# Kernel tuning notes

Measured on AMD Instinct MI355X. Metric: run time of the kernel, lower is better.

## Reference

```python
import jax, jax.numpy as jnp
from jax import lax
import numpy as np

DN = ('NCHW', 'OIHW', 'NCHW')

def lecun_tanh(z):
    return 1.7159 * jnp.tanh(0.666 * z)

def setup_inputs() -> dict:
    key = jax.random.key(0)
    ks = jax.random.split(key, 20)
    s = 0.02  # small init scale for numerical sanity
    inp = {
        'x_vis': jax.random.normal(ks[0], (32, 64, 3, 64, 64), jnp.float32),
        'hx': jnp.zeros((32, 64), jnp.float32),
        'conv1_w': jax.random.normal(ks[1], (32, 3, 4, 4), jnp.float32) * s,
        'conv1_b': jax.random.normal(ks[2], (32,), jnp.float32) * s,
        'conv2_w': jax.random.normal(ks[3], (64, 32, 4, 4), jnp.float32) * s,
        'conv2_b': jax.random.normal(ks[4], (64,), jnp.float32) * s,
        'bb_w': jax.random.normal(ks[5], (16448, 128), jnp.float32) * s,
        'bb_b': jax.random.normal(ks[6], (128,), jnp.float32) * s,
        'ff1_w': jax.random.normal(ks[7], (128, 64), jnp.float32) * s,
        'ff1_b': jax.random.normal(ks[8], (64,), jnp.float32) * s,
        'ff2_w': jax.random.normal(ks[9], (128, 64), jnp.float32) * s,
        'ff2_b': jax.random.normal(ks[10], (64,), jnp.float32) * s,
        'ta_w': jax.random.normal(ks[11], (128, 64), jnp.float32) * s,
        'ta_b': jax.random.normal(ks[12], (64,), jnp.float32) * s,
        'tb_w': jax.random.normal(ks[13], (128, 64), jnp.float32) * s,
        'tb_b': jax.random.normal(ks[14], (64,), jnp.float32) * s,
        'out_w': jax.random.normal(ks[15], (64, 8), jnp.float32) * s,
        'out_b': jax.random.normal(ks[16], (8,), jnp.float32) * s,
    }
    return inp

def reference(x_vis, hx, conv1_w, conv1_b, conv2_w, conv2_b, bb_w, bb_b,
              ff1_w, ff1_b, ff2_w, ff2_b, ta_w, ta_b, tb_w, tb_b, out_w, out_b):
    B, T, C, H, W = x_vis.shape
    x = x_vis.reshape(B * T, C, H, W)
    # Visual cortex: two stride-2 convs, k=4, p=1, ReLU
    x = jax.nn.relu(lax.conv_general_dilated(x, conv1_w, (2, 2), [(1, 1), (1, 1)],
                                             dimension_numbers=DN) + conv1_b[None, :, None, None])
    x = jax.nn.relu(lax.conv_general_dilated(x, conv2_w, (2, 2), [(1, 1), (1, 1)],
                                             dimension_numbers=DN) + conv2_b[None, :, None, None])
    feats = x.reshape(B, T, -1)  # (B, T, 16384)

    # CfC liquid core (ncps default mode, backbone_units=128, ts=1.0)
    ts = jnp.float32(1.0)
    def step(h, x_t):
        z = jnp.concatenate([x_t, h], axis=-1)            # (B, 16448)
        bb = lecun_tanh(z @ bb_w + bb_b)                   # (B, 128)
        ff1 = jnp.tanh(bb @ ff1_w + ff1_b)
        ff2 = jnp.tanh(bb @ ff2_w + ff2_b)
        t_interp = jax.nn.sigmoid((bb @ ta_w + ta_b) * ts + (bb @ tb_w + tb_b))
        h_new = ff1 * (1.0 - t_interp) + t_interp * ff2
        return h_new, h_new

    new_hx, outs = lax.scan(step, hx, jnp.swapaxes(feats, 0, 1))  # outs: (T, B, 64)
    r_out = jnp.swapaxes(outs, 0, 1)                               # (B, T, 64)
    logits = r_out @ out_w + out_b                                 # (B, T, 8)
    return logits, new_hx
```

## Files before the change

kernel.cpp:

```cpp
#include <hip/hip_runtime.h>
#include <stdint.h>


typedef unsigned short u16;
typedef unsigned int u32;

typedef float f32x4 __attribute__((ext_vector_type(4)));
typedef short s16x8 __attribute__((ext_vector_type(8)));
typedef __bf16 b16x8 __attribute__((ext_vector_type(8)));

template <typename V>
__device__ inline auto mfma_sel(V a, V b, f32x4 c, int)
    -> decltype(__builtin_amdgcn_mfma_f32_16x16x32_bf16(a, b, c, 0, 0, 0)) {
  return __builtin_amdgcn_mfma_f32_16x16x32_bf16(a, b, c, 0, 0, 0);
}
template <typename V>
__device__ inline f32x4 mfma_sel(V a, V b, f32x4 c, long) {
  union UU { V s; b16x8 b; };
  UU ua; ua.s = a;
  UU ub; ub.s = b;
  return __builtin_amdgcn_mfma_f32_16x16x32_bf16(ua.b, ub.b, c, 0, 0, 0);
}
__device__ inline f32x4 mfma16x16x32(s16x8 a, s16x8 b, f32x4 c) {
  return mfma_sel(a, b, c, 0);
}

__device__ inline float bf2f(u16 v) {
  union { u32 i; float f; } x; x.i = ((u32)v) << 16; return x.f;
}
__device__ inline u16 f2bf(float f) {
  union { float f; u32 i; } x; x.f = f;
  u32 i = x.i;
  i += 0x7fffu + ((i >> 16) & 1u);
  return (u16)(i >> 16);
}
__device__ inline void bf2x2(u32 u, float& lo, float& hi) {
  union { u32 i; float f; } a, b;
  a.i = u << 16; b.i = u & 0xffff0000u;
  lo = a.f; hi = b.f;
}
__device__ inline float ldf(int isbf, const void* p, size_t i) {
  return isbf ? bf2f(((const u16*)p)[i]) : ((const float*)p)[i];
}
__device__ inline u16 ldb(int isbf, const void* p, size_t i) {
  return isbf ? ((const u16*)p)[i] : f2bf(((const float*)p)[i]);
}
__device__ inline float fast_tanh(float x) {
  float ax = fabsf(x);
  float e = __expf(2.0f * ax);
  float t = 1.0f - 2.0f / (e + 1.0f);
  return copysignf(t, x);
}

__global__ __launch_bounds__(256)
void k_prep_all(const u32* __restrict__ bwords,
                const void* b1, const void* b2, const void* bbb,
                const void* f1b, const void* f2b, const void* tab,
                const void* tbb, const void* oww, const void* obb,
                const void* hx, const void* w1, const void* w2,
                const void* bw, const void* f1w, const void* f2w,
                const void* taw, const void* tbw,
                float* __restrict__ consts, u16* __restrict__ w1p,
                u16* __restrict__ w2c, u16* __restrict__ bbT,
                u16* __restrict__ HT, int* __restrict__ flag) {
  __shared__ u16 t[64][65];
  const int tid = threadIdx.x;
  const int b = blockIdx.x;
  const u32 wd = bwords[tid & 63];
  const u32 ex = (wd >> 7) & 0xFFu;
  unsigned long long m = __ballot(ex >= 100u && ex <= 126u);
  const int isbf = (__popcll(m) >= 32) ? 1 : 0;
  if (b == 0 && tid == 0) *flag = isbf;

  if (b < 12) {
    const int e = b * 256 + tid;
    if (e >= 3048) return;
    float v;
    if (e < 32)        v = ldf(isbf, b1, e);
    else if (e < 96)   v = ldf(isbf, b2, e - 32);
    else if (e < 224)  v = ldf(isbf, bbb, e - 96);
    else if (e < 288)  v = ldf(isbf, f1b, e - 224);
    else if (e < 352)  v = ldf(isbf, f2b, e - 288);
    else if (e < 416)  v = ldf(isbf, tab, e - 352);
    else if (e < 480)  v = ldf(isbf, tbb, e - 416);
    else if (e < 992)  v = ldf(isbf, oww, e - 480);
    else if (e < 1000) v = ldf(isbf, obb, e - 992);
    else               v = ldf(isbf, hx, e - 1000);
    consts[e] = v;
  } else if (b < 20) {
    const int e = (b - 12) * 256 + tid;
    const int k = e & 63, co = e >> 6;
    w1p[e] = (k < 48) ? ldb(isbf, w1, co * 48 + k) : (u16)0;
  } else if (b < 148) {
    const int e = (b - 20) * 256 + tid;
    w2c[e] = ldb(isbf, w2, e);
  } else if (b < 662) {
    const int idx = b - 148;
    const int k0 = (idx >> 1) * 64, j0 = (idx & 1) * 64;
    #pragma unroll
    for (int i = 0; i < 16; ++i) {
      int e = tid + 256 * i;
      int kl = e >> 6, jl = e & 63;
      t[kl][jl] = ldb(isbf, bw, (size_t)(k0 + kl) * 128 + j0 + jl);
    }
    __syncthreads();
    #pragma unroll
    for (int i = 0; i < 16; ++i) {
      int e = tid + 256 * i;
      int jl = e >> 6, kl = e & 63;
      bbT[(size_t)(j0 + jl) * 16448 + k0 + kl] = t[kl][jl];
    }
  } else {
    const int idx = b - 662;
    const int h = idx >> 1, i0 = (idx & 1) * 64;
    const void* W = (h == 0) ? f1w : (h == 1) ? f2w : (h == 2) ? taw : tbw;
    #pragma unroll
    for (int i = 0; i < 16; ++i) {
      int e = tid + 256 * i;
      int il = e >> 6, cl = e & 63;
      t[il][cl] = ldb(isbf, W, (i0 + il) * 64 + cl);
    }
    __syncthreads();
    #pragma unroll
    for (int i = 0; i < 16; ++i) {
      int e = tid + 256 * i;
      int cl = e >> 6, il = e & 63;
      HT[(h * 64 + cl) * 128 + i0 + il] = t[il][cl];
    }
  }
}

__global__ __launch_bounds__(512, 4)
void k_convs(const int* __restrict__ flagp, const void* __restrict__ x,
             const u16* __restrict__ w1p, const u16* __restrict__ w2c,
             const float* __restrict__ consts, u16* __restrict__ feats) {
  __shared__ u32 lx[16592];
  const int isbf = *flagp;
  const int n = blockIdx.x;
  const int tid = threadIdx.x;
  const int wv = tid >> 6, lane = tid & 63, quad = lane >> 4, l15 = lane & 15;

  for (int e = tid; e < 10064; e += 512) {
    int idx;
    if (e < 204) {
      const int pl = e / 68;
      const int rem = e - pl * 68;
      const int r = rem / 34;
      idx = pl * 2244 + r * (65 * 34) + (rem - r * 34);
    } else if (e < 272) {
      idx = 6732 + (e - 204);
    } else {
      idx = 6800 + (e - 272);
    }
    lx[idx] = 0u;
  }
  for (int e = tid; e < 3072; e += 512) {
    const int ci = e >> 10;
    const int rr = (e >> 4) & 63;
    const int tt = e & 15;
    u32* dst = &lx[(ci * 66 + rr + 1) * 34];
    if (!isbf) {
      const float* src = (const float*)x + (((size_t)n * 3 + ci) * 64 + rr) * 64 + 4 * tt;
      const f32x4 v = *(const f32x4*)src;
      const float pv = tt ? src[-1] : 0.f;
      dst[2 * tt]     = (u32)f2bf(pv)   | (((u32)f2bf(v[0])) << 16);
      dst[2 * tt + 1] = (u32)f2bf(v[1]) | (((u32)f2bf(v[2])) << 16);
      if (tt == 15) { dst[32] = (u32)f2bf(v[3]); dst[33] = 0u; }
    } else {
      const u16* src = (const u16*)x + (((size_t)n * 3 + ci) * 64 + rr) * 64 + 4 * tt;
      const u16 pv = tt ? src[-1] : (u16)0;
      dst[2 * tt]     = (u32)pv | (((u32)src[0]) << 16);
      dst[2 * tt + 1] = (u32)src[1] | (((u32)src[2]) << 16);
      if (tt == 15) { dst[32] = (u32)src[3]; dst[33] = 0u; }
    }
  }
  __syncthreads();

  f32x4 acc2[8];
  #pragma unroll
  for (int rr = 0; rr < 8; ++rr) acc2[rr] = f32x4{0.f, 0.f, 0.f, 0.f};

  const int khb = (quad & 1) * 2;
  const int cih = quad >> 1;
  const int mt = wv & 3;
  const int og = wv >> 2;
  u16* lp = (u16*)lx;

  #pragma unroll
  for (int h = 0; h < 2; ++h) {
    const s16x8 af0 = *(const s16x8*)(w1p + (h * 16 + l15) * 64 + quad * 8);
    const s16x8 af1 = *(const s16x8*)(w1p + (h * 16 + l15) * 64 + 32 + quad * 8);
    #pragma unroll
    for (int i = 0; i < 8; ++i) {
      const int nt = wv * 8 + i;
      const int oh = nt >> 1;
      const int ob = (nt & 1) * 16;
      f32x4 a1acc = f32x4{0.f, 0.f, 0.f, 0.f};
      {
        const int base = (cih * 66 + 2 * oh + khb) * 34 + ob + l15;
        union { u32 u[4]; s16x8 v; } bf;
        bf.u[0] = lx[base];
        bf.u[1] = lx[base + 1];
        bf.u[2] = lx[base + 34];
        bf.u[3] = lx[base + 35];
        a1acc = mfma16x16x32(af0, bf.v, a1acc);
      }
      {
        const int ci1 = 2 + cih;
        const int base = (ci1 < 3) ? ((ci1 * 66 + 2 * oh + khb) * 34 + ob + l15)
                                   : (6732 + ob + l15);
        union { u32 u[4]; s16x8 v; } bf;
        bf.u[0] = lx[base];
        bf.u[1] = lx[base + 1];
        bf.u[2] = lx[base + 34];
        bf.u[3] = lx[base + 35];
        a1acc = mfma16x16x32(af1, bf.v, a1acc);
      }
      #pragma unroll
      for (int r = 0; r < 4; ++r) {
        const int co = quad * 4 + r;
        float v = a1acc[r] + consts[h * 16 + co];
        v = v > 0.f ? v : 0.f;
        lp[(6800 + (co * 34 + oh + 1) * 18) * 2 + ob + l15 + 1] = f2bf(v);
      }
    }
    __syncthreads();
    #pragma unroll
    for (int kst = 0; kst < 8; ++kst) {
      const int kglob = h * 8 + kst;
      const s16x8 afr =
          *(const s16x8*)(w2c + (mt * 16 + l15) * 512 + kglob * 32 + quad * 8);
      const int ci = kst * 2 + cih;
      #pragma unroll
      for (int rr = 0; rr < 8; ++rr) {
        const int row1 = 2 * (og * 8 + rr) + khb;
        const int base = 6800 + (ci * 34 + row1) * 18 + l15;
        union { u32 u[4]; s16x8 v; } bf;
        bf.u[0] = lx[base];
        bf.u[1] = lx[base + 1];
        bf.u[2] = lx[base + 18];
        bf.u[3] = lx[base + 19];
        acc2[rr] = mfma16x16x32(afr, bf.v, acc2[rr]);
      }
    }
    if (h == 0) __syncthreads();
  }
  #pragma unroll
  for (int rr = 0; rr < 8; ++rr) {
    const int oh = og * 8 + rr;
    #pragma unroll
    for (int r = 0; r < 4; ++r) {
      const int co = mt * 16 + quad * 4 + r;
      const float bias = consts[32 + co];
      float v = acc2[rr][r] + bias;
      v = v > 0.f ? v : 0.f;
      feats[(size_t)n * 16384 + co * 256 + oh * 16 + l15] = f2bf(v);
    }
  }
}

__global__ __launch_bounds__(256)
void k_xb(const u16* __restrict__ feats, const u16* __restrict__ bbT,
          float* __restrict__ xbp) {
  const int m0 = blockIdx.x * 64;
  const int kc = blockIdx.y;
  const int kc0 = kc * 1024;
  const int tid = threadIdx.x;
  const int w = tid >> 6, lane = tid & 63, quad = lane >> 4, l15 = lane & 15;
  f32x4 acc[4][2];
  #pragma unroll
  for (int mt = 0; mt < 4; ++mt)
    #pragma unroll
    for (int i = 0; i < 2; ++i) acc[mt][i] = f32x4{0.f, 0.f, 0.f, 0.f};
  #pragma unroll 4
  for (int kst = 0; kst < 32; ++kst) {
    const int k = kc0 + kst * 32 + quad * 8;
    s16x8 afrag[4], bfrag[2];
    #pragma unroll
    for (int mt = 0; mt < 4; ++mt)
      afrag[mt] = *(const s16x8*)(feats + (size_t)(m0 + mt * 16 + l15) * 16384 + k);
    #pragma unroll
    for (int i = 0; i < 2; ++i)
      bfrag[i] = *(const s16x8*)(bbT + (size_t)((w * 2 + i) * 16 + l15) * 16448 + k);
    #pragma unroll
    for (int mt = 0; mt < 4; ++mt)
      #pragma unroll
      for (int i = 0; i < 2; ++i)
        acc[mt][i] = mfma16x16x32(afrag[mt], bfrag[i], acc[mt][i]);
  }
  float* dst = xbp + (size_t)kc * 262144;
  #pragma unroll
  for (int mt = 0; mt < 4; ++mt)
    #pragma unroll
    for (int i = 0; i < 2; ++i) {
      const int j = (w * 2 + i) * 16 + l15;
      #pragma unroll
      for (int r = 0; r < 4; ++r) {
        const int m = m0 + mt * 16 + quad * 4 + r;
        dst[m * 128 + j] = acc[mt][i][r];
      }
    }
}

__global__ __launch_bounds__(256)
void k_xbsum(const float* __restrict__ xbp, float* __restrict__ xb) {
  const int e = blockIdx.x * 256 + threadIdx.x;
  float s = 0.f;
  #pragma unroll
  for (int kc = 0; kc < 16; ++kc) s += xbp[(size_t)kc * 262144 + e];
  xb[e] = s;
}

__global__ __launch_bounds__(256, 1)
void k_rec(const int* __restrict__ flagp, const float* __restrict__ xb,
           const u16* __restrict__ bbT, const u16* __restrict__ HT,
           const float* __restrict__ consts, float* __restrict__ rout,
           void* __restrict__ outv) {
  __shared__ float xbl[64 * 128];
  __shared__ float h[64];
  __shared__ float bbv[128];
  __shared__ float heads[256];
  const int isbf = *flagp;
  const int b = blockIdx.x;
  const int tid = threadIdx.x;
  {
    const float* src = xb + (size_t)b * 64 * 128;
    #pragma unroll
    for (int q = 0; q < 32; ++q) xbl[q * 256 + tid] = src[q * 256 + tid];
  }
  float w1r[64];
  if (tid < 128) {
    const u32* src = (const u32*)(bbT + (size_t)tid * 16448 + 16384);
    #pragma unroll
    for (int q = 0; q < 32; ++q) bf2x2(src[q], w1r[2 * q], w1r[2 * q + 1]);
  }
  float w2r[128];
  {
    const u32* src = (const u32*)(HT + tid * 128);
    #pragma unroll
    for (int q = 0; q < 64; ++q) bf2x2(src[q], w2r[2 * q], w2r[2 * q + 1]);
  }
  const float hbias = consts[224 + tid];
  const float bbias = (tid < 128) ? consts[96 + tid] : 0.f;
  if (tid < 64) h[tid] = consts[1000 + b * 64 + tid];
  __syncthreads();
  for (int t = 0; t < 64; ++t) {
    if (tid < 128) {
      float p0 = 0.f, p1 = 0.f, p2 = 0.f, p3 = 0.f;
      #pragma unroll
      for (int q = 0; q < 16; ++q) {
        p0 += h[4 * q + 0] * w1r[4 * q + 0];
        p1 += h[4 * q + 1] * w1r[4 * q + 1];
        p2 += h[4 * q + 2] * w1r[4 * q + 2];
        p3 += h[4 * q + 3] * w1r[4 * q + 3];
      }
      const float s = (p0 + p1) + (p2 + p3) + xbl[t * 128 + tid] + bbias;
      bbv[tid] = 1.7159f * fast_tanh(0.666f * s);
    }
    __syncthreads();
    float c0 = 0.f, c1 = 0.f, c2 = 0.f, c3 = 0.f;
    #pragma unroll
    for (int q = 0; q < 32; ++q) {
      c0 += bbv[4 * q + 0] * w2r[4 * q + 0];
      c1 += bbv[4 * q + 1] * w2r[4 * q + 1];
      c2 += bbv[4 * q + 2] * w2r[4 * q + 2];
      c3 += bbv[4 * q + 3] * w2r[4 * q + 3];
    }
    heads[tid] = (c0 + c1) + (c2 + c3) + hbias;
    __syncthreads();
    if (tid < 64) {
      const float ff1 = fast_tanh(heads[tid]);
      const float ff2 = fast_tanh(heads[64 + tid]);
      const float ti = 1.f / (1.f + __expf(-(heads[128 + tid] + heads[192 + tid])));
      const float hn = ff1 * (1.f - ti) + ti * ff2;
      h[tid] = hn;
      rout[((size_t)b * 64 + t) * 64 + tid] = hn;
    }
    __syncthreads();
  }
  if (tid < 64) {
    if (isbf) ((u16*)outv)[16384 + b * 64 + tid] = f2bf(h[tid]);
    else      ((float*)outv)[16384 + b * 64 + tid] = h[tid];
  }
}

__global__ __launch_bounds__(256)
void k_logits(const int* __restrict__ flagp, const float* __restrict__ rout,
              const float* __restrict__ consts, void* __restrict__ outv) {
  __shared__ float W[512];
  __shared__ float Bv[8];
  const int isbf = *flagp;
  const int tid = threadIdx.x;
  for (int e = tid; e < 512; e += 256) W[e] = consts[480 + e];
  if (tid < 8) Bv[tid] = consts[992 + tid];
  __syncthreads();
  const int bt = blockIdx.x * 256 + tid;
  float acc[8];
  #pragma unroll
  for (int c = 0; c < 8; ++c) acc[c] = Bv[c];
  const f32x4* r = (const f32x4*)(rout + (size_t)bt * 64);
  #pragma unroll
  for (int q = 0; q < 16; ++q) {
    f32x4 v = r[q];
    #pragma unroll
    for (int u = 0; u < 4; ++u) {
      const float rv = v[u];
      const int i = 4 * q + u;
      #pragma unroll
      for (int c = 0; c < 8; ++c) acc[c] += rv * W[i * 8 + c];
    }
  }
  if (isbf) {
    u32 pk[4];
    #pragma unroll
    for (int c = 0; c < 4; ++c)
      pk[c] = (u32)f2bf(acc[2 * c]) | ((u32)f2bf(acc[2 * c + 1]) << 16);
    *(uint4*)((u16*)outv + (size_t)bt * 8) = *(const uint4*)pk;
  } else {
    float* o = (float*)outv + (size_t)bt * 8;
    *(f32x4*)o = f32x4{acc[0], acc[1], acc[2], acc[3]};
    *(f32x4*)(o + 4) = f32x4{acc[4], acc[5], acc[6], acc[7]};
  }
}

extern "C" void kernel_launch(void* const* d_in, const int* in_sizes, int n_in,
                              void* d_out, int out_size, void* d_ws, size_t ws_size,
                              hipStream_t stream) {
  const void* x   = d_in[0];
  const void* hx  = d_in[1];
  const void* w1  = d_in[2];
  const void* b1  = d_in[3];
  const void* w2  = d_in[4];
  const void* b2  = d_in[5];
  const void* bbw = d_in[6];
  const void* bbb = d_in[7];
  const void* f1w = d_in[8];
  const void* f1b = d_in[9];
  const void* f2w = d_in[10];
  const void* f2b = d_in[11];
  const void* taw = d_in[12];
  const void* tab = d_in[13];
  const void* tbw = d_in[14];
  const void* tbb = d_in[15];
  const void* oww = d_in[16];
  const void* obb = d_in[17];

  char* ws = (char*)d_ws;
  float* xbp   = (float*)(ws);
  u16*   feats = (u16*)(ws + 150994944);
  u16*   bbT   = (u16*)(ws + 218103808);
  u16*   HT    = (u16*)(ws + 222314496);
  u16*   w1p   = (u16*)(ws + 222380032);
  u16*   w2c   = (u16*)(ws + 222384128);
  float* xb    = (float*)(ws + 222449664);
  float* rout  = (float*)(ws + 223498240);
  float* consts= (float*)(ws + 224022528);
  int*   flag  = (int*)(ws + 224034816);

  k_prep_all<<<670, 256, 0, stream>>>((const u32*)bbw, b1, b2, bbb, f1b, f2b,
                                      tab, tbb, oww, obb, hx, w1, w2, bbw,
                                      f1w, f2w, taw, tbw,
                                      consts, w1p, w2c, bbT, HT, flag);
  k_convs<<<2048, 512, 0, stream>>>(flag, x, w1p, w2c, consts, feats);
  k_xb<<<dim3(32, 16), 256, 0, stream>>>(feats, bbT, xbp);
  k_xbsum<<<1024, 256, 0, stream>>>(xbp, xb);
  k_rec<<<32, 256, 0, stream>>>(flag, xb, bbT, HT, consts, rout, d_out);
  k_logits<<<8, 256, 0, stream>>>(flag, rout, consts, d_out);
}
```

Baseline: 422.6 us.

## Split recurrent matvecs across 512 threads with shuffle reductions, removing a barrier

The sequential recurrence kernel now uses 512 threads per batch row. Each thread computes a partial dot product over a slice of K, and the partials are combined with cross-lane shuffles instead of one thread looping over the full K. The four head outputs are gathered by shuffles within a wave, which removes the shared heads array and one __syncthreads per timestep. This aims to shorten the serial per-step latency of the 64-step loop, at the cost of extra shuffle traffic and vectorized LDS reads.

```diff
diff --git a/kernel.cpp b/kernel.cpp
--- a/kernel.cpp
+++ b/kernel.cpp
@@ -311,70 +311,90 @@
   xb[e] = s;
 }
 
-__global__ __launch_bounds__(256, 1)
+__global__ __launch_bounds__(512, 1)
 void k_rec(const int* __restrict__ flagp, const float* __restrict__ xb,
            const u16* __restrict__ bbT, const u16* __restrict__ HT,
            const float* __restrict__ consts, float* __restrict__ rout,
            void* __restrict__ outv) {
   __shared__ float xbl[64 * 128];
-  __shared__ float h[64];
-  __shared__ float bbv[128];
-  __shared__ float heads[256];
+  __shared__ f32x4 h4[16];
+  __shared__ f32x4 bb4[32];
   const int isbf = *flagp;
   const int b = blockIdx.x;
   const int tid = threadIdx.x;
+  const int w = tid >> 6;
+  const int l = tid & 63;
+  float* h = (float*)h4;
+  float* bbv = (float*)bb4;
+
   {
     const float* src = xb + (size_t)b * 64 * 128;
     #pragma unroll
-    for (int q = 0; q < 32; ++q) xbl[q * 256 + tid] = src[q * 256 + tid];
-  }
-  float w1r[64];
-  if (tid < 128) {
-    const u32* src = (const u32*)(bbT + (size_t)tid * 16448 + 16384);
-    #pragma unroll
-    for (int q = 0; q < 32; ++q) bf2x2(src[q], w1r[2 * q], w1r[2 * q + 1]);
-  }
-  float w2r[128];
+    for (int q = 0; q < 16; ++q) xbl[q * 512 + tid] = src[q * 512 + tid];
+  }
+  const int jo = w * 16 + (l & 15);
+  const int kh1 = l >> 4;
+  float w1r[16];
   {
-    const u32* src = (const u32*)(HT + tid * 128);
-    #pragma unroll
-    for (int q = 0; q < 64; ++q) bf2x2(src[q], w2r[2 * q], w2r[2 * q + 1]);
-  }
-  const float hbias = consts[224 + tid];
-  const float bbias = (tid < 128) ? consts[96 + tid] : 0.f;
+    const u32* src = (const u32*)(bbT + (size_t)jo * 16448 + 16384 + kh1 * 16);
+    #pragma unroll
+    for (int q = 0; q < 8; ++q) bf2x2(src[q], w1r[2 * q], w1r[2 * q + 1]);
+  }
+  const int g = (l >> 3) & 3;
+  const int u8 = l & 7;
+  const int jo2 = g * 64 + w * 8 + u8;
+  const int kh2 = l >> 5;
+  float w2r[64];
+  {
+    const u32* src = (const u32*)(HT + jo2 * 128 + kh2 * 64);
+    #pragma unroll
+    for (int q = 0; q < 32; ++q) bf2x2(src[q], w2r[2 * q], w2r[2 * q + 1]);
+  }
+  const float bbias = consts[96 + jo];
+  const float hbias = consts[224 + jo2];
   if (tid < 64) h[tid] = consts[1000 + b * 64 + tid];
   __syncthreads();
+
   for (int t = 0; t < 64; ++t) {
-    if (tid < 128) {
-      float p0 = 0.f, p1 = 0.f, p2 = 0.f, p3 = 0.f;
-      #pragma unroll
-      for (int q = 0; q < 16; ++q) {
-        p0 += h[4 * q + 0] * w1r[4 * q + 0];
-        p1 += h[4 * q + 1] * w1r[4 * q + 1];
-        p2 += h[4 * q + 2] * w1r[4 * q + 2];
-        p3 += h[4 * q + 3] * w1r[4 * q + 3];
-      }
-      const float s = (p0 + p1) + (p2 + p3) + xbl[t * 128 + tid] + bbias;
-      bbv[tid] = 1.7159f * fast_tanh(0.666f * s);
+    float p = 0.f;
+    #pragma unroll
+    for (int q = 0; q < 4; ++q) {
+      const f32x4 hv = h4[kh1 * 4 + q];
+      p += hv[0] * w1r[4 * q + 0];
+      p += hv[1] * w1r[4 * q + 1];
+      p += hv[2] * w1r[4 * q + 2];
+      p += hv[3] * w1r[4 * q + 3];
+    }
+    p += __shfl_xor(p, 16);
+    p += __shfl_xor(p, 32);
+    if (l < 16) {
+      const float s = p + xbl[t * 128 + jo] + bbias;
+      bbv[jo] = 1.7159f * fast_tanh(0.666f * s);
     }
     __syncthreads();
-    float c0 = 0.f, c1 = 0.f, c2 = 0.f, c3 = 0.f;
-    #pragma unroll
-    for (int q = 0; q < 32; ++q) {
-      c0 += bbv[4 * q + 0] * w2r[4 * q + 0];
-      c1 += bbv[4 * q + 1] * w2r[4 * q + 1];
-      c2 += bbv[4 * q + 2] * w2r[4 * q + 2];
-      c3 += bbv[4 * q + 3] * w2r[4 * q + 3];
-    }
-    heads[tid] = (c0 + c1) + (c2 + c3) + hbias;
-    __syncthreads();
-    if (tid < 64) {
-      const float ff1 = fast_tanh(heads[tid]);
-      const float ff2 = fast_tanh(heads[64 + tid]);
-      const float ti = 1.f / (1.f + __expf(-(heads[128 + tid] + heads[192 + tid])));
+    float p2 = 0.f;
+    #pragma unroll
+    for (int q = 0; q < 16; ++q) {
+      const f32x4 bv = bb4[kh2 * 16 + q];
+      p2 += bv[0] * w2r[4 * q + 0];
+      p2 += bv[1] * w2r[4 * q + 1];
+      p2 += bv[2] * w2r[4 * q + 2];
+      p2 += bv[3] * w2r[4 * q + 3];
+    }
+    p2 += __shfl_xor(p2, 32);
+    p2 += hbias;
+    const float v0 = __shfl(p2, u8);
+    const float v1 = __shfl(p2, 8 + u8);
+    const float v2 = __shfl(p2, 16 + u8);
+    const float v3 = __shfl(p2, 24 + u8);
+    if (l < 8) {
+      const float ff1 = fast_tanh(v0);
+      const float ff2 = fast_tanh(v1);
+      const float ti = 1.f / (1.f + __expf(-(v2 + v3)));
       const float hn = ff1 * (1.f - ti) + ti * ff2;
-      h[tid] = hn;
-      rout[((size_t)b * 64 + t) * 64 + tid] = hn;
+      const int unit = w * 8 + l;
+      h[unit] = hn;
+      rout[((size_t)b * 64 + t) * 64 + unit] = hn;
     }
     __syncthreads();
   }
@@ -464,6 +484,6 @@
   k_convs<<<2048, 512, 0, stream>>>(flag, x, w1p, w2c, consts, feats);
   k_xb<<<dim3(32, 16), 256, 0, stream>>>(feats, bbT, xbp);
   k_xbsum<<<1024, 256, 0, stream>>>(xbp, xb);
-  k_rec<<<32, 256, 0, stream>>>(flag, xb, bbT, HT, consts, rout, d_out);
+  k_rec<<<32, 512, 0, stream>>>(flag, xb, bbT, HT, consts, rout, d_out);
   k_logits<<<8, 256, 0, stream>>>(flag, rout, consts, d_out);
 }
```

Result: faster. 383.1 us (-9.3%).
